# Optimization experiments

Measured on AMD Instinct MI355X. Metric: run time of the kernel, lower is better.

The kernel has to match this reference:

```python
import jax, jax.numpy as jnp
from jax import lax
import numpy as np
import math

EPS = 1e-6

def _np(a, s=1.0):
    return np.asarray(a, dtype=np.float32) * np.float32(s)

def _gabor(theta, sigma=1.1, lambd=3.0, gamma=0.65):
    c = np.arange(-2, 3, dtype=np.float32)
    yy, xx = np.meshgrid(c, c, indexing='ij')
    xt = xx * math.cos(theta) + yy * math.sin(theta)
    yt = -xx * math.sin(theta) + yy * math.cos(theta)
    k = np.exp(-(xt**2 + gamma**2 * yt**2) / (2.0 * sigma**2)) * np.cos(2.0 * math.pi * xt / lambd)
    k = k - k.mean()
    return (k / max(np.abs(k).sum(), 1e-6)).astype(np.float32)

def _dct_like(u=2, v=2, size=5):
    c = np.arange(size, dtype=np.float32)
    yy, xx = np.meshgrid(c, c, indexing='ij')
    k = np.cos(math.pi*(2*xx+1)*u/(2*size)) * np.cos(math.pi*(2*yy+1)*v/(2*size))
    k = k - k.mean()
    return (k / max(np.abs(k).sum(), 1e-6)).astype(np.float32)

# stacked 3x3 stencils: laplacian, hess_xx, hess_yy, hess_xy, sobel_x, sobel_y, diag_main, diag_anti, checkerboard
_K3 = np.stack([
    _np([[0,1,0],[1,-4,1],[0,1,0]]),
    _np([[0,0,0],[1,-2,1],[0,0,0]]),
    _np([[0,1,0],[0,-2,0],[0,1,0]]),
    _np([[1,0,-1],[0,0,0],[-1,0,1]], 0.25),
    _np([[-1,0,1],[-2,0,2],[-1,0,1]], 0.125),
    _np([[-1,-2,-1],[0,0,0],[1,2,1]], 0.125),
    _np([[-2,-1,0],[-1,0,1],[0,1,2]], 0.125),
    _np([[0,1,2],[-1,0,1],[-2,-1,0]], 0.125),
    _np([[1,-1,1],[-1,1,-1],[1,-1,1]], 1.0/9.0),
])[:, None]

_Z5 = np.zeros((5,5), np.float32)

def _row5(vals):
    k = _Z5.copy(); k[2, :] = vals; return k

def _col5(vals):
    k = _Z5.copy(); k[:, 2] = vals; return k

# stacked 5x5 stencils: ha_second_h, ha_second_v, ha_green_h, ha_green_v, mhc_green, stripe_x, stripe_y, gabor45, gabor135, dct
_K5 = np.stack([
    _row5([-0.5, 0.0, 1.0, 0.0, -0.5]),
    _col5([-0.5, 0.0, 1.0, 0.0, -0.5]),
    _row5([-0.25, 0.5, 0.5, 0.5, -0.25]),
    _col5([-0.25, 0.5, 0.5, 0.5, -0.25]),
    _np([[0,0,-1,0,0],[0,0,2,0,0],[-1,2,4,2,-1],[0,0,2,0,0],[0,0,-1,0,0]], 0.125),
    _row5([0.25, -1.0, 1.5, -1.0, 0.25]),
    _col5([0.25, -1.0, 1.5, -1.0, 0.25]),
    _gabor(math.pi/4.0),
    _gabor(3.0*math.pi/4.0),
    _dct_like(),
])[:, None]

_SMOOTH5 = (_np([[1,2,3,2,1],[2,4,6,4,2],[3,6,9,6,3],[2,4,6,4,2],[1,2,3,2,1]]) / np.float32(81.0))[None, None]

K3 = jnp.asarray(_K3)
K5 = jnp.asarray(_K5)
SMOOTH5 = jnp.asarray(_SMOOTH5)

def _masks(H, W):
    # gbrg pattern
    z = lambda: np.zeros((1, 1, H, W), np.float32)
    r, b, gr, gb, row, col = z(), z(), z(), z(), z(), z()
    row[:, :, 1::2, :] = 1.0
    col[:, :, :, 1::2] = 1.0
    gb[:, :, 0::2, 0::2] = 1.0
    b[:, :, 0::2, 1::2] = 1.0
    r[:, :, 1::2, 0::2] = 1.0
    gr[:, :, 1::2, 1::2] = 1.0
    g = gr + gb
    return tuple(jnp.asarray(a) for a in (r, g, b, gr, gb, row, col))

def _pad(x, ph, pw):
    return jnp.pad(x, ((0, 0), (0, 0), (ph, ph), (pw, pw)), mode='reflect')

def _conv_same(x, k, groups=1):
    kh, kw = k.shape[-2:]
    return lax.conv_general_dilated(_pad(x, kh // 2, kw // 2), k.astype(x.dtype), (1, 1), 'VALID',
                                    dimension_numbers=('NCHW', 'OIHW', 'NCHW'),
                                    feature_group_count=groups)

def _avg_same(x, kh, kw):
    k = jnp.full((1, 1, kh, kw), 1.0 / (kh * kw), x.dtype)
    return _conv_same(x, k)

def _forward(bayer):
    B, _, H, W = bayer.shape
    r, g, b, gr, gb, row, col = _masks(H, W)
    c3 = _conv_same(bayer, K3)  # [B,9,H,W]
    lap, hxx, hyy, hxy, gx, gy, gdm, gda, chk = jnp.split(c3, 9, axis=1)
    c5 = _conv_same(bayer, K5)  # [B,10,H,W]
    hsh, hsv, hgh, hgv, mhcf, stx, sty, g45, g135, dctp = jnp.split(c5, 10, axis=1)
    # morphological gradient: 3x3 max - min (reflect-padded)
    xp = _pad(bayer, 1, 1)
    mgrad = (lax.reduce_window(xp, -jnp.inf, lax.max, (1, 1, 3, 3), (1, 1, 1, 1), 'VALID')
             - lax.reduce_window(xp, jnp.inf, lax.min, (1, 1, 3, 3), (1, 1, 1, 1), 'VALID'))
    gmag = jnp.sqrt(gx * gx + gy * gy + EPS)
    # structure tensor (3x3 box smoothing of gradient outer products)
    jxx = _avg_same(gx * gx, 3, 3)
    jyy = _avg_same(gy * gy, 3, 3)
    jxy = _avg_same(gx * gy, 3, 3)
    tr = jxx + jyy
    lam_gap = jnp.sqrt((jxx - jyy) ** 2 + 4.0 * jxy * jxy + EPS)
    coherence = lam_gap / (tr + EPS)
    anisotropy = (jxx - jyy) / (tr + EPS)
    ha_dis = jnp.abs(hgh - hgv)
    res_h = bayer - hgh
    res_v = bayer - hgv
    res_eh = _avg_same(res_h * res_h, 3, 3)
    res_ev = _avg_same(res_v * res_v, 3, 3)
    dgd = jnp.abs(gx) - jnp.abs(gy)
    dsd = jnp.abs(hxx) - jnp.abs(hyy)
    # 1x5 / 5x1 line variances
    mh = _avg_same(bayer, 1, 5)
    mv = _avg_same(bayer, 5, 1)
    lvh = jnp.maximum(_avg_same(bayer * bayer, 1, 5) - mh * mh, 0.0)
    lvv = jnp.maximum(_avg_same(bayer * bayer, 5, 1) - mv * mv, 0.0)
    lvd = lvh - lvv
    dconf = jnp.abs(lvd) / (lvh + lvv + EPS)
    # normalized sparse fills (smooth5 of masked signal / smooth5 of mask)
    mstack = jnp.concatenate([r, g, b, gr, gb], axis=1)  # [1,5,H,W]
    sig = bayer * mstack  # [B,5,H,W]
    ks = jnp.tile(SMOOTH5, (5, 1, 1, 1))
    num = _conv_same(sig, ks, groups=5)
    den = jnp.maximum(_conv_same(mstack, ks, groups=5), EPS)
    rf, gf, bf, grf, gbf = jnp.split(num / den, 5, axis=1)
    rg = rf - gf
    bg = bf - gf
    gpd = grf - gbf
    mhc = jnp.where(g > 0.5, bayer, mhcf)
    mhc_ha = mhc - 0.5 * (hgh + hgv)
    rres = (bayer - mhc) * r
    bres = (bayer - mhc) * b
    chk_e = _avg_same(chk * chk, 3, 3)
    str_e = _avg_same(stx * stx + sty * sty, 3, 3)
    lmean = _avg_same(bayer, 3, 3)
    lvar = jnp.maximum(_avg_same(bayer * bayer, 3, 3) - lmean * lmean, 0.0)
    gen = _avg_same(gx * gx + gy * gy, 3, 3)
    bm = lambda m: jnp.broadcast_to(m, bayer.shape)
    feats = [bm(r), bm(g), bm(b), bm(gr), bm(gb), bm(row), bm(col),
             lap, hxx, hyy, hxy, mgrad, gx, gy, gdm, gda, gmag,
             coherence, anisotropy, hsh, hsv, hgh, hgv, ha_dis,
             res_h, res_v, res_eh, res_ev, dgd, dsd, lvh, lvv, lvd, dconf,
             rg, bg, gpd, mhc, mhc_ha, rres, bres,
             stx, sty, chk, g45, g135, dctp, chk_e, str_e, lmean, lvar, gen]
    return jnp.concatenate(feats, axis=1)  # [B,52,H,W]

def setup_inputs() -> dict:
    key = jax.random.key(0)
    bayer = jax.random.uniform(key, (2, 1, 768, 768), dtype=jnp.float32)
    return {"bayer": bayer}

def reference(bayer):
    return _forward(bayer)
```

## Files before the change

kernel.cpp:

```cpp
#include <hip/hip_runtime.h>
#include <math.h>

#define H_ 768
#define W_ 768
#define TY 16
#define TX 64
#define NTHREADS 256
#define EPS_ 1e-6f

__device__ __forceinline__ int refl(int c, int n) {
    c = c < 0 ? -c : c;
    c = c >= n ? 2 * n - 2 - c : c;
    return c;
}

__global__ __launch_bounds__(NTHREADS)
void bayer_feat(const float* __restrict__ in, float* __restrict__ out) {
    const int bz  = blockIdx.z;
    const int gy0 = blockIdx.y * TY;
    const int gx0 = blockIdx.x * TX;
    const int tid = threadIdx.x;
    const float* src = in + (size_t)bz * (H_ * W_);

    __shared__ float sB[TY + 6][TX + 7];
    __shared__ float sE[7][TY + 2][TX + 2];

    for (int i = tid; i < (TY + 6) * (TX + 6); i += NTHREADS) {
        int r = i / (TX + 6), c = i - r * (TX + 6);
        sB[r][c] = src[refl(gy0 - 3 + r, H_) * W_ + refl(gx0 - 3 + c, W_)];
    }
    __syncthreads();

    for (int i = tid; i < (TY + 2) * (TX + 2); i += NTHREADS) {
        int ey = i / (TX + 2), ex = i - ey * (TX + 2);
        int sy = refl(gy0 - 1 + ey, H_) - gy0 + 3;
        int sx = refl(gx0 - 1 + ex, W_) - gx0 + 3;
        float a00 = sB[sy-1][sx-1], a01 = sB[sy-1][sx], a02 = sB[sy-1][sx+1];
        float a10 = sB[sy  ][sx-1], a11 = sB[sy  ][sx], a12 = sB[sy  ][sx+1];
        float a20 = sB[sy+1][sx-1], a21 = sB[sy+1][sx], a22 = sB[sy+1][sx+1];
        float l2 = sB[sy][sx-2], r2 = sB[sy][sx+2];
        float u2 = sB[sy-2][sx], d2 = sB[sy+2][sx];
        sE[0][ey][ex] = 0.125f * (-a00 + a02 - 2.f*a10 + 2.f*a12 - a20 + a22);
        sE[1][ey][ex] = 0.125f * (-a00 - 2.f*a01 - a02 + a20 + 2.f*a21 + a22);
        sE[2][ey][ex] = -0.25f*(l2 + r2) + 0.5f*(a10 + a11 + a12);
        sE[3][ey][ex] = -0.25f*(u2 + d2) + 0.5f*(a01 + a11 + a21);
        sE[4][ey][ex] = (a00 - a01 + a02 - a10 + a11 - a12 + a20 - a21 + a22) * (1.f/9.f);
        sE[5][ey][ex] = 0.25f*(l2 + r2) - (a10 + a12) + 1.5f*a11;
        sE[6][ey][ex] = 0.25f*(u2 + d2) - (a01 + a21) + 1.5f*a11;
    }
    __syncthreads();

    const int tx = tid & 63;
    const int ty = tid >> 6;
    const size_t HW = (size_t)H_ * W_;
    float* outb = out + (size_t)bz * 52 * HW;

    const float G45[5][5] = {
        {-0.002092f, -0.015195f, -0.063321f, -0.002285f,  0.036511f},
        {-0.015195f, -0.086304f,  0.003803f,  0.119456f, -0.002285f},
        {-0.063321f,  0.003803f,  0.172851f,  0.003803f, -0.063321f},
        {-0.002285f,  0.119456f,  0.003803f, -0.086304f, -0.015195f},
        { 0.036511f, -0.002285f, -0.063321f, -0.015195f, -0.002092f}
    };
    const float ADC[5] = {0.25f, -0.09549150f, -0.30901699f, -0.09549150f, 0.25f};
    const float inv9 = 1.f / 9.f;

    for (int k = 0; k < 4; ++k) {
        const int ly = ty * 4 + k;
        const int lx = tx;
        const int gy = gy0 + ly, gx = gx0 + lx;
        const int sy = ly + 3, sx = lx + 3;
        const int ey = ly + 1, ex = lx + 1;
        const int py = gy & 1, px = gx & 1;

        float a[5][5];
#pragma unroll
        for (int dy = 0; dy < 5; ++dy)
#pragma unroll
            for (int dx = 0; dx < 5; ++dx)
                a[dy][dx] = sB[sy - 2 + dy][sx - 2 + dx];

#define A_(dy, dx) a[(dy) + 2][(dx) + 2]
        float* po = outb + (size_t)gy * W_ + gx;
#define ST(c, v) po[(size_t)(c) * HW] = (v)

        ST(0, (float)(py & (px ^ 1)));
        ST(1, (float)(py == px));
        ST(2, (float)((py ^ 1) & px));
        ST(3, (float)(py & px));
        ST(4, (float)((py ^ 1) & (px ^ 1)));
        ST(5, (float)py);
        ST(6, (float)px);

        float lap = A_(-1,0) + A_(0,-1) - 4.f*A_(0,0) + A_(0,1) + A_(1,0);
        float hxx = A_(0,-1) - 2.f*A_(0,0) + A_(0,1);
        float hyy = A_(-1,0) - 2.f*A_(0,0) + A_(1,0);
        float hxy = 0.25f*(A_(-1,-1) - A_(-1,1) - A_(1,-1) + A_(1,1));
        ST(7, lap); ST(8, hxx); ST(9, hyy); ST(10, hxy);

        float mxv = A_(-1,-1), mnv = A_(-1,-1);
#pragma unroll
        for (int dy = -1; dy <= 1; ++dy)
#pragma unroll
            for (int dx = -1; dx <= 1; ++dx) {
                float v = A_(dy, dx);
                mxv = fmaxf(mxv, v); mnv = fminf(mnv, v);
            }
        ST(11, mxv - mnv);

        float gxv = sE[0][ey][ex], gyv = sE[1][ey][ex];
        ST(12, gxv); ST(13, gyv);
        float gdm = 0.125f*(-2.f*A_(-1,-1) - A_(-1,0) - A_(0,-1) + A_(0,1) + A_(1,0) + 2.f*A_(1,1));
        float gda = 0.125f*(A_(-1,0) + 2.f*A_(-1,1) - A_(0,-1) + A_(0,1) - 2.f*A_(1,-1) - A_(1,0));
        ST(14, gdm); ST(15, gda);
        ST(16, sqrtf(gxv*gxv + gyv*gyv + EPS_));

        float jxx = 0.f, jyy = 0.f, jxy = 0.f, reh = 0.f, rev = 0.f, cke = 0.f, ste = 0.f;
#pragma unroll
        for (int dy = -1; dy <= 1; ++dy)
#pragma unroll
            for (int dx = -1; dx <= 1; ++dx) {
                float gxn = sE[0][ey+dy][ex+dx];
                float gyn = sE[1][ey+dy][ex+dx];
                jxx += gxn*gxn; jyy += gyn*gyn; jxy += gxn*gyn;
                float bn = A_(dy, dx);
                float rh = bn - sE[2][ey+dy][ex+dx];
                float rv = bn - sE[3][ey+dy][ex+dx];
                reh += rh*rh; rev += rv*rv;
                float ckn = sE[4][ey+dy][ex+dx];
                cke += ckn*ckn;
                float sxn = sE[5][ey+dy][ex+dx], syn = sE[6][ey+dy][ex+dx];
                ste += sxn*sxn + syn*syn;
            }
        jxx *= inv9; jyy *= inv9; jxy *= inv9;
        float trc = jxx + jyy;
        float lam = sqrtf((jxx - jyy)*(jxx - jyy) + 4.f*jxy*jxy + EPS_);
        ST(17, lam / (trc + EPS_));
        ST(18, (jxx - jyy) / (trc + EPS_));

        float hsh = -0.5f*(A_(0,-2) + A_(0,2)) + A_(0,0);
        float hsv = -0.5f*(A_(-2,0) + A_(2,0)) + A_(0,0);
        ST(19, hsh); ST(20, hsv);
        float hghv = sE[2][ey][ex], hgvv = sE[3][ey][ex];
        ST(21, hghv); ST(22, hgvv);
        ST(23, fabsf(hghv - hgvv));
        float ctr = A_(0,0);
        ST(24, ctr - hghv); ST(25, ctr - hgvv);
        ST(26, reh * inv9); ST(27, rev * inv9);
        ST(28, fabsf(gxv) - fabsf(gyv));
        ST(29, fabsf(hxx) - fabsf(hyy));

        float sh = A_(0,-2)+A_(0,-1)+A_(0,0)+A_(0,1)+A_(0,2);
        float qh = A_(0,-2)*A_(0,-2)+A_(0,-1)*A_(0,-1)+A_(0,0)*A_(0,0)+A_(0,1)*A_(0,1)+A_(0,2)*A_(0,2);
        float sv = A_(-2,0)+A_(-1,0)+A_(0,0)+A_(1,0)+A_(2,0);
        float qv = A_(-2,0)*A_(-2,0)+A_(-1,0)*A_(-1,0)+A_(0,0)*A_(0,0)+A_(1,0)*A_(1,0)+A_(2,0)*A_(2,0);
        float mh = sh * 0.2f, mv = sv * 0.2f;
        float lvh = fmaxf(qh*0.2f - mh*mh, 0.f);
        float lvv = fmaxf(qv*0.2f - mv*mv, 0.f);
        ST(30, lvh); ST(31, lvv);
        float lvd = lvh - lvv;
        ST(32, lvd);
        ST(33, fabsf(lvd) / (lvh + lvv + EPS_));

        float cEE, cOE, cEO, cOO;
        {
            float rEv[5], rOv[5];
#pragma unroll
            for (int dy = 0; dy < 5; ++dy) {
                float e0 = a[dy][0] + 3.f*a[dy][2] + a[dy][4];
                float e1 = 2.f*(a[dy][1] + a[dy][3]);
                rEv[dy] = px ? e1 : e0;
                rOv[dy] = px ? e0 : e1;
            }
            float t0 = rEv[0] + 3.f*rEv[2] + rEv[4];
            float t1 = 2.f*(rEv[1] + rEv[3]);
            float t2 = rOv[0] + 3.f*rOv[2] + rOv[4];
            float t3 = 2.f*(rOv[1] + rOv[3]);
            cEE = py ? t1 : t0;
            cOE = py ? t0 : t1;
            cEO = py ? t3 : t2;
            cOO = py ? t2 : t3;
        }
        float Sy_e = py ? 4.f : 5.f, Sx_e = px ? 4.f : 5.f;
        float Sy_o = 9.f - Sy_e,     Sx_o = 9.f - Sx_e;
        float rfv  = cOE / (Sy_o * Sx_e);
        float bfv  = cEO / (Sy_e * Sx_o);
        float grfv = cOO / (Sy_o * Sx_o);
        float gbfv = cEE / (Sy_e * Sx_e);
        float gfv  = (cEE + cOO) / (Sy_e * Sx_e + Sy_o * Sx_o);
        ST(34, rfv - gfv);
        ST(35, bfv - gfv);
        ST(36, grfv - gbfv);

        float mhcf = 0.125f*(-A_(-2,0) + 2.f*A_(-1,0) - A_(0,-2) + 2.f*A_(0,-1) + 4.f*A_(0,0)
                             + 2.f*A_(0,1) - A_(0,2) + 2.f*A_(1,0) - A_(2,0));
        float mhc = (py == px) ? ctr : mhcf;
        ST(37, mhc);
        ST(38, mhc - 0.5f*(hghv + hgvv));
        ST(39, (py & (px ^ 1)) ? (ctr - mhc) : 0.f);
        ST(40, ((py ^ 1) & px) ? (ctr - mhc) : 0.f);

        ST(41, sE[5][ey][ex]); ST(42, sE[6][ey][ex]); ST(43, sE[4][ey][ex]);

        float s45 = 0.f, s135 = 0.f;
#pragma unroll
        for (int dy = 0; dy < 5; ++dy)
#pragma unroll
            for (int dx = 0; dx < 5; ++dx) {
                s45  += G45[dy][dx]     * a[dy][dx];
                s135 += G45[dy][4 - dx] * a[dy][dx];
            }
        ST(44, s45); ST(45, s135);

        float dctp = 0.f;
#pragma unroll
        for (int dy = 0; dy < 5; ++dy) {
            float t = ADC[0]*a[dy][0] + ADC[1]*a[dy][1] + ADC[2]*a[dy][2] + ADC[3]*a[dy][3] + ADC[4]*a[dy][4];
            dctp += ADC[dy] * t;
        }
        ST(46, dctp);

        ST(47, cke * inv9);
        ST(48, ste * inv9);

        float s3 = 0.f, q3 = 0.f;
#pragma unroll
        for (int dy = -1; dy <= 1; ++dy)
#pragma unroll
            for (int dx = -1; dx <= 1; ++dx) { float v = A_(dy, dx); s3 += v; q3 += v*v; }
        float lmean = s3 * inv9;
        ST(49, lmean);
        ST(50, fmaxf(q3 * inv9 - lmean*lmean, 0.f));
        ST(51, trc);

#undef A_
#undef ST
    }
}

extern "C" void kernel_launch(void* const* d_in, const int* in_sizes, int n_in,
                              void* d_out, int out_size, void* d_ws, size_t ws_size,
                              hipStream_t stream) {
    (void)n_in; (void)d_ws; (void)ws_size; (void)out_size;
    const float* bayer = (const float*)d_in[0];
    float* out = (float*)d_out;
    const int B = in_sizes[0] / (H_ * W_);
    dim3 grid(W_ / TX, H_ / TY, B);
    bayer_feat<<<grid, NTHREADS, 0, stream>>>(bayer, out);
}
```

Before: 51.32 us.

## Compute four adjacent pixels per thread with vectorized nontemporal float4 stores

Each thread now handles four horizontally adjacent pixels of one row instead of four rows of one pixel. All 52 output channels are written as 16-byte nontemporal float4 stores, and the 5x8 register window plus sliding sE reads are shared across the four pixels. Per-pixel parity branches become constant lane patterns, and divisions are replaced by fast reciprocals or precomputed constants. The change targets store-instruction count and write bandwidth of this output-bound kernel, at the cost of more registers per thread and slightly different rounding from the approximate reciprocal.

Result: slower. 56.21 us (+9.5%).

```diff
diff --git a/kernel.cpp b/kernel.cpp
--- a/kernel.cpp
+++ b/kernel.cpp
@@ -8,10 +8,26 @@
 #define NTHREADS 256
 #define EPS_ 1e-6f
 
+typedef float f4 __attribute__((ext_vector_type(4)));
+
+__device__ __forceinline__ f4 mk4(float x, float y, float z, float w){ f4 r; r.x=x; r.y=y; r.z=z; r.w=w; return r; }
+__device__ __forceinline__ f4 sp(float s){ return mk4(s,s,s,s); }
+__device__ __forceinline__ f4 max4(f4 a, f4 b){ return mk4(fmaxf(a.x,b.x),fmaxf(a.y,b.y),fmaxf(a.z,b.z),fmaxf(a.w,b.w)); }
+__device__ __forceinline__ f4 min4(f4 a, f4 b){ return mk4(fminf(a.x,b.x),fminf(a.y,b.y),fminf(a.z,b.z),fminf(a.w,b.w)); }
+__device__ __forceinline__ f4 sqrt4(f4 a){ return mk4(sqrtf(a.x),sqrtf(a.y),sqrtf(a.z),sqrtf(a.w)); }
+__device__ __forceinline__ f4 abs4(f4 a){ return mk4(fabsf(a.x),fabsf(a.y),fabsf(a.z),fabsf(a.w)); }
+__device__ __forceinline__ float rcp1(float x){
+#if __has_builtin(__builtin_amdgcn_rcpf)
+    return __builtin_amdgcn_rcpf(x);
+#else
+    return 1.0f / x;
+#endif
+}
+__device__ __forceinline__ f4 rcp4(f4 a){ return mk4(rcp1(a.x),rcp1(a.y),rcp1(a.z),rcp1(a.w)); }
+
 __device__ __forceinline__ int refl(int c, int n) {
     c = c < 0 ? -c : c;
-    c = c >= n ? 2 * n - 2 - c : c;
-    return c;
+    return c >= n ? 2 * n - 2 - c : c;
 }
 
 __global__ __launch_bounds__(NTHREADS)
@@ -23,7 +39,7 @@
     const float* src = in + (size_t)bz * (H_ * W_);
 
     __shared__ float sB[TY + 6][TX + 7];
-    __shared__ float sE[7][TY + 2][TX + 2];
+    __shared__ float sE[7][TY + 2][TX + 3];
 
     for (int i = tid; i < (TY + 6) * (TX + 6); i += NTHREADS) {
         int r = i / (TX + 6), c = i - r * (TX + 6);
@@ -50,192 +66,203 @@
     }
     __syncthreads();
 
-    const int tx = tid & 63;
-    const int ty = tid >> 6;
+    const int lq  = tid & 15;
+    const int ly  = tid >> 4;
+    const int lx4 = lq * 4;
+    const int gy  = gy0 + ly, gx = gx0 + lx4;
+    const int py  = gy & 1;
+    const int syc = ly + 3;
+    const int ey  = ly + 1;
+    const int exb = lx4 + 1;
     const size_t HW = (size_t)H_ * W_;
-    float* outb = out + (size_t)bz * 52 * HW;
-
-    const float G45[5][5] = {
-        {-0.002092f, -0.015195f, -0.063321f, -0.002285f,  0.036511f},
-        {-0.015195f, -0.086304f,  0.003803f,  0.119456f, -0.002285f},
-        {-0.063321f,  0.003803f,  0.172851f,  0.003803f, -0.063321f},
-        {-0.002285f,  0.119456f,  0.003803f, -0.086304f, -0.015195f},
-        { 0.036511f, -0.002285f, -0.063321f, -0.015195f, -0.002092f}
-    };
-    const float ADC[5] = {0.25f, -0.09549150f, -0.30901699f, -0.09549150f, 0.25f};
+    float* po = out + (size_t)bz * 52 * HW + (size_t)gy * W_ + gx;
+
+#define ST(c, v) __builtin_nontemporal_store((v), (f4*)(po + (size_t)(c) * HW))
+
+    float a[5][8];
+#pragma unroll
+    for (int r = 0; r < 5; ++r)
+#pragma unroll
+        for (int i = 0; i < 8; ++i)
+            a[r][i] = sB[syc - 2 + r][lx4 + 1 + i];
+
+#define AV(r, i) mk4(a[r][i], a[r][(i)+1], a[r][(i)+2], a[r][(i)+3])
+#define SL(arr, o) mk4(arr[o], arr[(o)+1], arr[(o)+2], arr[(o)+3])
+
+    const f4 zero4 = sp(0.f);
+    const f4 ev01  = mk4(0,1,0,1);
+    const f4 ev10  = mk4(1,0,1,0);
     const float inv9 = 1.f / 9.f;
 
-    for (int k = 0; k < 4; ++k) {
-        const int ly = ty * 4 + k;
-        const int lx = tx;
-        const int gy = gy0 + ly, gx = gx0 + lx;
-        const int sy = ly + 3, sx = lx + 3;
-        const int ey = ly + 1, ex = lx + 1;
-        const int py = gy & 1, px = gx & 1;
-
-        float a[5][5];
-#pragma unroll
-        for (int dy = 0; dy < 5; ++dy)
-#pragma unroll
-            for (int dx = 0; dx < 5; ++dx)
-                a[dy][dx] = sB[sy - 2 + dy][sx - 2 + dx];
-
-#define A_(dy, dx) a[(dy) + 2][(dx) + 2]
-        float* po = outb + (size_t)gy * W_ + gx;
-#define ST(c, v) po[(size_t)(c) * HW] = (v)
-
-        ST(0, (float)(py & (px ^ 1)));
-        ST(1, (float)(py == px));
-        ST(2, (float)((py ^ 1) & px));
-        ST(3, (float)(py & px));
-        ST(4, (float)((py ^ 1) & (px ^ 1)));
-        ST(5, (float)py);
-        ST(6, (float)px);
-
-        float lap = A_(-1,0) + A_(0,-1) - 4.f*A_(0,0) + A_(0,1) + A_(1,0);
-        float hxx = A_(0,-1) - 2.f*A_(0,0) + A_(0,1);
-        float hyy = A_(-1,0) - 2.f*A_(0,0) + A_(1,0);
-        float hxy = 0.25f*(A_(-1,-1) - A_(-1,1) - A_(1,-1) + A_(1,1));
-        ST(7, lap); ST(8, hxx); ST(9, hyy); ST(10, hxy);
-
-        float mxv = A_(-1,-1), mnv = A_(-1,-1);
-#pragma unroll
-        for (int dy = -1; dy <= 1; ++dy)
-#pragma unroll
-            for (int dx = -1; dx <= 1; ++dx) {
-                float v = A_(dy, dx);
-                mxv = fmaxf(mxv, v); mnv = fminf(mnv, v);
+    ST(0, py ? ev10 : zero4);
+    ST(1, py ? ev01 : ev10);
+    ST(2, py ? zero4 : ev01);
+    ST(3, py ? ev01 : zero4);
+    ST(4, py ? zero4 : ev10);
+    ST(5, sp((float)py));
+    ST(6, ev01);
+
+    f4 jxx = zero4, jyy = zero4, jxy = zero4, reh = zero4, rev = zero4, cke = zero4, ste = zero4;
+    f4 gxv = zero4, gyv = zero4, hghv = zero4, hgvv = zero4, chkv = zero4, stxv = zero4, styv = zero4;
+#pragma unroll
+    for (int dy = -1; dy <= 1; ++dy) {
+        float g_[6], h_[6], hh_[6], hv_[6], ck_[6], sx_[6], sy_[6];
+#pragma unroll
+        for (int j = 0; j < 6; ++j) {
+            g_[j]  = sE[0][ey+dy][exb-1+j];
+            h_[j]  = sE[1][ey+dy][exb-1+j];
+            hh_[j] = sE[2][ey+dy][exb-1+j];
+            hv_[j] = sE[3][ey+dy][exb-1+j];
+            ck_[j] = sE[4][ey+dy][exb-1+j];
+            sx_[j] = sE[5][ey+dy][exb-1+j];
+            sy_[j] = sE[6][ey+dy][exb-1+j];
+        }
+        f4 bm_ = AV(dy+2, 1), b0_ = AV(dy+2, 2), bp_ = AV(dy+2, 3);
+#pragma unroll
+        for (int o = 0; o < 3; ++o) {
+            f4 q = SL(g_, o), w = SL(h_, o);
+            jxx += q*q; jyy += w*w; jxy += q*w;
+            if (dy == 0 && o == 1) { gxv = q; gyv = w; }
+            f4 bb = (o == 0) ? bm_ : (o == 1 ? b0_ : bp_);
+            f4 rh = bb - SL(hh_, o); reh += rh*rh;
+            f4 rv = bb - SL(hv_, o); rev += rv*rv;
+            if (dy == 0 && o == 1) { hghv = SL(hh_, 1); hgvv = SL(hv_, 1); }
+            f4 cc = SL(ck_, o); cke += cc*cc;
+            if (dy == 0 && o == 1) chkv = cc;
+            f4 s1 = SL(sx_, o), s2 = SL(sy_, o);
+            ste += s1*s1 + s2*s2;
+            if (dy == 0 && o == 1) { stxv = s1; styv = s2; }
+        }
+    }
+    jxx = jxx * sp(inv9); jyy = jyy * sp(inv9); jxy = jxy * sp(inv9);
+
+    f4 ctr = AV(2,2);
+    ST(12, gxv); ST(13, gyv);
+    ST(16, sqrt4(gxv*gxv + gyv*gyv + sp(EPS_)));
+    f4 trc = jxx + jyy;
+    f4 dj  = jxx - jyy;
+    f4 lam = sqrt4(dj*dj + sp(4.f)*jxy*jxy + sp(EPS_));
+    f4 itr = rcp4(trc + sp(EPS_));
+    ST(17, lam * itr);
+    ST(18, dj * itr);
+    ST(21, hghv); ST(22, hgvv);
+    ST(23, abs4(hghv - hgvv));
+    ST(24, ctr - hghv); ST(25, ctr - hgvv);
+    ST(26, reh * sp(inv9)); ST(27, rev * sp(inv9));
+    ST(28, abs4(gxv) - abs4(gyv));
+    ST(41, stxv); ST(42, styv); ST(43, chkv);
+    ST(47, cke * sp(inv9)); ST(48, ste * sp(inv9));
+    ST(51, trc);
+
+    f4 lap = AV(1,2) + AV(2,1) - sp(4.f)*ctr + AV(2,3) + AV(3,2);
+    f4 hxx = AV(2,1) - sp(2.f)*ctr + AV(2,3);
+    f4 hyy = AV(1,2) - sp(2.f)*ctr + AV(3,2);
+    f4 hxy = sp(0.25f)*(AV(1,1) - AV(1,3) - AV(3,1) + AV(3,3));
+    ST(7, lap); ST(8, hxx); ST(9, hyy); ST(10, hxy);
+    ST(29, abs4(hxx) - abs4(hyy));
+
+    {
+        f4 mx = AV(1,1), mn = mx;
+#pragma unroll
+        for (int r = 1; r <= 3; ++r)
+#pragma unroll
+            for (int i = 1; i <= 3; ++i) { f4 v = AV(r,i); mx = max4(mx, v); mn = min4(mn, v); }
+        ST(11, mx - mn);
+    }
+
+    ST(14, sp(0.125f)*(sp(-2.f)*AV(1,1) - AV(1,2) - AV(2,1) + AV(2,3) + AV(3,2) + sp(2.f)*AV(3,3)));
+    ST(15, sp(0.125f)*(AV(1,2) + sp(2.f)*AV(1,3) - AV(2,1) + AV(2,3) - sp(2.f)*AV(3,1) - AV(3,2)));
+    ST(19, sp(-0.5f)*(AV(2,0) + AV(2,4)) + ctr);
+    ST(20, sp(-0.5f)*(AV(0,2) + AV(4,2)) + ctr);
+
+    {
+        f4 sh = AV(2,0)+AV(2,1)+AV(2,2)+AV(2,3)+AV(2,4);
+        f4 qh = AV(2,0)*AV(2,0)+AV(2,1)*AV(2,1)+AV(2,2)*AV(2,2)+AV(2,3)*AV(2,3)+AV(2,4)*AV(2,4);
+        f4 sv_ = AV(0,2)+AV(1,2)+AV(2,2)+AV(3,2)+AV(4,2);
+        f4 qv_ = AV(0,2)*AV(0,2)+AV(1,2)*AV(1,2)+AV(2,2)*AV(2,2)+AV(3,2)*AV(3,2)+AV(4,2)*AV(4,2);
+        f4 mh = sh * sp(0.2f), mv = sv_ * sp(0.2f);
+        f4 lvh = max4(qh*sp(0.2f) - mh*mh, zero4);
+        f4 lvv = max4(qv_*sp(0.2f) - mv*mv, zero4);
+        ST(30, lvh); ST(31, lvv);
+        f4 lvd = lvh - lvv;
+        ST(32, lvd);
+        ST(33, abs4(lvd) * rcp4(lvh + lvv + sp(EPS_)));
+    }
+
+    {
+        f4 t0 = zero4, t1 = zero4, t2 = zero4, t3 = zero4;
+#pragma unroll
+        for (int r = 0; r < 5; ++r) {
+            f4 E = AV(r,0) + sp(3.f)*AV(r,2) + AV(r,4);
+            f4 O = sp(2.f)*(AV(r,1) + AV(r,3));
+            f4 rE = mk4(E.x, O.y, E.z, O.w);
+            f4 rO = mk4(O.x, E.y, O.z, E.w);
+            if (r == 0 || r == 4)      { t0 += rE;          t2 += rO; }
+            else if (r == 2)           { t0 += sp(3.f)*rE;  t2 += sp(3.f)*rO; }
+            else                       { t1 += sp(2.f)*rE;  t3 += sp(2.f)*rO; }
+        }
+        f4 cEE = py ? t1 : t0, cOE = py ? t0 : t1, cEO = py ? t3 : t2, cOO = py ? t2 : t3;
+        const f4 inv_r  = py ? mk4(0.04f,0.05f,0.04f,0.05f)     : mk4(0.05f,0.0625f,0.05f,0.0625f);
+        const f4 inv_b  = py ? mk4(0.0625f,0.05f,0.0625f,0.05f) : mk4(0.05f,0.04f,0.05f,0.04f);
+        const f4 inv_gr = py ? mk4(0.05f,0.04f,0.05f,0.04f)     : mk4(0.0625f,0.05f,0.0625f,0.05f);
+        const f4 inv_gb = py ? mk4(0.05f,0.0625f,0.05f,0.0625f) : mk4(0.04f,0.05f,0.04f,0.05f);
+        const f4 inv_g  = py ? mk4(1.f/40.f,1.f/41.f,1.f/40.f,1.f/41.f)
+                             : mk4(1.f/41.f,1.f/40.f,1.f/41.f,1.f/40.f);
+        f4 rfv = cOE*inv_r, bfv = cEO*inv_b, grfv = cOO*inv_gr, gbfv = cEE*inv_gb;
+        f4 gfv = (cEE + cOO)*inv_g;
+        ST(34, rfv - gfv); ST(35, bfv - gfv); ST(36, grfv - gbfv);
+    }
+
+    {
+        f4 mhcf = sp(0.125f)*( -AV(0,2) + sp(2.f)*AV(1,2) - AV(2,0) + sp(2.f)*AV(2,1) + sp(4.f)*ctr
+                               + sp(2.f)*AV(2,3) - AV(2,4) + sp(2.f)*AV(3,2) - AV(4,2) );
+        f4 mhc = py ? mk4(mhcf.x, ctr.y, mhcf.z, ctr.w) : mk4(ctr.x, mhcf.y, ctr.z, mhcf.w);
+        ST(37, mhc);
+        ST(38, mhc - sp(0.5f)*(hghv + hgvv));
+        f4 dif = ctr - mhc;
+        ST(39, dif * (py ? ev10 : zero4));
+        ST(40, dif * (py ? zero4 : ev01));
+    }
+
+    {
+        const float G45[5][5] = {
+            {-0.002092f, -0.015195f, -0.063321f, -0.002285f,  0.036511f},
+            {-0.015195f, -0.086304f,  0.003803f,  0.119456f, -0.002285f},
+            {-0.063321f,  0.003803f,  0.172851f,  0.003803f, -0.063321f},
+            {-0.002285f,  0.119456f,  0.003803f, -0.086304f, -0.015195f},
+            { 0.036511f, -0.002285f, -0.063321f, -0.015195f, -0.002092f}
+        };
+        const float ADC[5] = {0.25f, -0.09549150f, -0.30901699f, -0.09549150f, 0.25f};
+        f4 s45 = zero4, s135 = zero4, dct = zero4;
+#pragma unroll
+        for (int r = 0; r < 5; ++r) {
+            f4 t = zero4;
+#pragma unroll
+            for (int i = 0; i < 5; ++i) {
+                f4 v = AV(r, i);
+                s45  += sp(G45[r][i])     * v;
+                s135 += sp(G45[r][4 - i]) * v;
+                t    += sp(ADC[i])        * v;
             }
-        ST(11, mxv - mnv);
-
-        float gxv = sE[0][ey][ex], gyv = sE[1][ey][ex];
-        ST(12, gxv); ST(13, gyv);
-        float gdm = 0.125f*(-2.f*A_(-1,-1) - A_(-1,0) - A_(0,-1) + A_(0,1) + A_(1,0) + 2.f*A_(1,1));
-        float gda = 0.125f*(A_(-1,0) + 2.f*A_(-1,1) - A_(0,-1) + A_(0,1) - 2.f*A_(1,-1) - A_(1,0));
-        ST(14, gdm); ST(15, gda);
-        ST(16, sqrtf(gxv*gxv + gyv*gyv + EPS_));
-
-        float jxx = 0.f, jyy = 0.f, jxy = 0.f, reh = 0.f, rev = 0.f, cke = 0.f, ste = 0.f;
-#pragma unroll
-        for (int dy = -1; dy <= 1; ++dy)
-#pragma unroll
-            for (int dx = -1; dx <= 1; ++dx) {
-                float gxn = sE[0][ey+dy][ex+dx];
-                float gyn = sE[1][ey+dy][ex+dx];
-                jxx += gxn*gxn; jyy += gyn*gyn; jxy += gxn*gyn;
-                float bn = A_(dy, dx);
-                float rh = bn - sE[2][ey+dy][ex+dx];
-                float rv = bn - sE[3][ey+dy][ex+dx];
-                reh += rh*rh; rev += rv*rv;
-                float ckn = sE[4][ey+dy][ex+dx];
-                cke += ckn*ckn;
-                float sxn = sE[5][ey+dy][ex+dx], syn = sE[6][ey+dy][ex+dx];
-                ste += sxn*sxn + syn*syn;
-            }
-        jxx *= inv9; jyy *= inv9; jxy *= inv9;
-        float trc = jxx + jyy;
-        float lam = sqrtf((jxx - jyy)*(jxx - jyy) + 4.f*jxy*jxy + EPS_);
-        ST(17, lam / (trc + EPS_));
-        ST(18, (jxx - jyy) / (trc + EPS_));
-
-        float hsh = -0.5f*(A_(0,-2) + A_(0,2)) + A_(0,0);
-        float hsv = -0.5f*(A_(-2,0) + A_(2,0)) + A_(0,0);
-        ST(19, hsh); ST(20, hsv);
-        float hghv = sE[2][ey][ex], hgvv = sE[3][ey][ex];
-        ST(21, hghv); ST(22, hgvv);
-        ST(23, fabsf(hghv - hgvv));
-        float ctr = A_(0,0);
-        ST(24, ctr - hghv); ST(25, ctr - hgvv);
-        ST(26, reh * inv9); ST(27, rev * inv9);
-        ST(28, fabsf(gxv) - fabsf(gyv));
-        ST(29, fabsf(hxx) - fabsf(hyy));
-
-        float sh = A_(0,-2)+A_(0,-1)+A_(0,0)+A_(0,1)+A_(0,2);
-        float qh = A_(0,-2)*A_(0,-2)+A_(0,-1)*A_(0,-1)+A_(0,0)*A_(0,0)+A_(0,1)*A_(0,1)+A_(0,2)*A_(0,2);
-        float sv = A_(-2,0)+A_(-1,0)+A_(0,0)+A_(1,0)+A_(2,0);
-        float qv = A_(-2,0)*A_(-2,0)+A_(-1,0)*A_(-1,0)+A_(0,0)*A_(0,0)+A_(1,0)*A_(1,0)+A_(2,0)*A_(2,0);
-        float mh = sh * 0.2f, mv = sv * 0.2f;
-        float lvh = fmaxf(qh*0.2f - mh*mh, 0.f);
-        float lvv = fmaxf(qv*0.2f - mv*mv, 0.f);
-        ST(30, lvh); ST(31, lvv);
-        float lvd = lvh - lvv;
-        ST(32, lvd);
-        ST(33, fabsf(lvd) / (lvh + lvv + EPS_));
-
-        float cEE, cOE, cEO, cOO;
-        {
-            float rEv[5], rOv[5];
-#pragma unroll
-            for (int dy = 0; dy < 5; ++dy) {
-                float e0 = a[dy][0] + 3.f*a[dy][2] + a[dy][4];
-                float e1 = 2.f*(a[dy][1] + a[dy][3]);
-                rEv[dy] = px ? e1 : e0;
-                rOv[dy] = px ? e0 : e1;
-            }
-            float t0 = rEv[0] + 3.f*rEv[2] + rEv[4];
-            float t1 = 2.f*(rEv[1] + rEv[3]);
-            float t2 = rOv[0] + 3.f*rOv[2] + rOv[4];
-            float t3 = 2.f*(rOv[1] + rOv[3]);
-            cEE = py ? t1 : t0;
-            cOE = py ? t0 : t1;
-            cEO = py ? t3 : t2;
-            cOO = py ? t2 : t3;
-        }
-        float Sy_e = py ? 4.f : 5.f, Sx_e = px ? 4.f : 5.f;
-        float Sy_o = 9.f - Sy_e,     Sx_o = 9.f - Sx_e;
-        float rfv  = cOE / (Sy_o * Sx_e);
-        float bfv  = cEO / (Sy_e * Sx_o);
-        float grfv = cOO / (Sy_o * Sx_o);
-        float gbfv = cEE / (Sy_e * Sx_e);
-        float gfv  = (cEE + cOO) / (Sy_e * Sx_e + Sy_o * Sx_o);
-        ST(34, rfv - gfv);
-        ST(35, bfv - gfv);
-        ST(36, grfv - gbfv);
-
-        float mhcf = 0.125f*(-A_(-2,0) + 2.f*A_(-1,0) - A_(0,-2) + 2.f*A_(0,-1) + 4.f*A_(0,0)
-                             + 2.f*A_(0,1) - A_(0,2) + 2.f*A_(1,0) - A_(2,0));
-        float mhc = (py == px) ? ctr : mhcf;
-        ST(37, mhc);
-        ST(38, mhc - 0.5f*(hghv + hgvv));
-        ST(39, (py & (px ^ 1)) ? (ctr - mhc) : 0.f);
-        ST(40, ((py ^ 1) & px) ? (ctr - mhc) : 0.f);
-
-        ST(41, sE[5][ey][ex]); ST(42, sE[6][ey][ex]); ST(43, sE[4][ey][ex]);
-
-        float s45 = 0.f, s135 = 0.f;
-#pragma unroll
-        for (int dy = 0; dy < 5; ++dy)
-#pragma unroll
-            for (int dx = 0; dx < 5; ++dx) {
-                s45  += G45[dy][dx]     * a[dy][dx];
-                s135 += G45[dy][4 - dx] * a[dy][dx];
-            }
-        ST(44, s45); ST(45, s135);
-
-        float dctp = 0.f;
-#pragma unroll
-        for (int dy = 0; dy < 5; ++dy) {
-            float t = ADC[0]*a[dy][0] + ADC[1]*a[dy][1] + ADC[2]*a[dy][2] + ADC[3]*a[dy][3] + ADC[4]*a[dy][4];
-            dctp += ADC[dy] * t;
-        }
-        ST(46, dctp);
-
-        ST(47, cke * inv9);
-        ST(48, ste * inv9);
-
-        float s3 = 0.f, q3 = 0.f;
-#pragma unroll
-        for (int dy = -1; dy <= 1; ++dy)
-#pragma unroll
-            for (int dx = -1; dx <= 1; ++dx) { float v = A_(dy, dx); s3 += v; q3 += v*v; }
-        float lmean = s3 * inv9;
+            dct += sp(ADC[r]) * t;
+        }
+        ST(44, s45); ST(45, s135); ST(46, dct);
+    }
+
+    {
+        f4 s3 = zero4, q3 = zero4;
+#pragma unroll
+        for (int r = 1; r <= 3; ++r)
+#pragma unroll
+            for (int i = 1; i <= 3; ++i) { f4 v = AV(r,i); s3 += v; q3 += v*v; }
+        f4 lmean = s3 * sp(inv9);
         ST(49, lmean);
-        ST(50, fmaxf(q3 * inv9 - lmean*lmean, 0.f));
-        ST(51, trc);
-
-#undef A_
+        ST(50, max4(q3*sp(inv9) - lmean*lmean, zero4));
+    }
+
 #undef ST
-    }
+#undef AV
+#undef SL
 }
 
 extern "C" void kernel_launch(void* const* d_in, const int* in_sizes, int n_in,
```
